# Performance work log

Measured on AMD Instinct MI355X. Metric: run time of the kernel, lower is better.

The kernel has to match this reference:

```python
import jax, jax.numpy as jnp
import numpy as np

# Static module configuration (RT-DETR defaults, 640x640 input pyramid)
SPATIAL_SHAPES = ((80, 80), (40, 40), (20, 20))
N_HEADS = 8
N_LEVELS = 3
N_POINTS = 4
D_MODEL = 256
HEAD_DIM = D_MODEL // N_HEADS
OFFSET_SCALE = 0.5
LP = N_LEVELS * N_POINTS


def setup_inputs() -> dict:
    key = jax.random.key(0)
    ks = jax.random.split(key, 10)
    B, Q = 16, 300
    S = sum(h * w for h, w in SPATIAL_SHAPES)  # 8400

    def w(k, shape, scale=0.02):
        return jax.random.normal(k, shape, jnp.float32) * scale

    return {
        "hidden_states": jax.random.normal(ks[0], (B, Q, D_MODEL), jnp.float32),
        "encoder_hidden_states": jax.random.normal(ks[1], (B, S, D_MODEL), jnp.float32),
        # (cx, cy, w, h) boxes in (0,1); 4-coordinate RTDETRv2 path
        "reference_points": jax.random.uniform(ks[2], (B, Q, 1, 4), jnp.float32, 0.1, 0.9),
        "w_value": w(ks[3], (D_MODEL, D_MODEL)),
        "b_value": jnp.zeros((D_MODEL,), jnp.float32),
        "w_offsets": w(ks[4], (N_HEADS * LP * 2, D_MODEL)),
        "b_offsets": w(ks[5], (N_HEADS * LP * 2,), 0.5),
        "w_attn": w(ks[6], (N_HEADS * LP, D_MODEL)),
        "b_attn": jnp.zeros((N_HEADS * LP,), jnp.float32),
        "w_out": w(ks[7], (D_MODEL, D_MODEL)),
        "b_out": jnp.zeros((D_MODEL,), jnp.float32),
    }


def _bilinear_sample(img, gx, gy):
    """grid_sample(mode=bilinear, padding_mode=zeros, align_corners=False).
    img: [N, C, H, W]; gx, gy: [N, Q, P] absolute pixel coords (already W*loc-0.5).
    Returns [N, Q, P, C]."""
    N, C, H, W = img.shape
    x0 = jnp.floor(gx)
    y0 = jnp.floor(gy)
    x1 = x0 + 1.0
    y1 = y0 + 1.0
    wx1 = gx - x0
    wx0 = 1.0 - wx1
    wy1 = gy - y0
    wy0 = 1.0 - wy1
    b = jnp.arange(N)[:, None, None]

    def gather(ix, iy):
        valid = (ix >= 0) & (ix < W) & (iy >= 0) & (iy < H)
        ixc = jnp.clip(ix, 0, W - 1).astype(jnp.int32)
        iyc = jnp.clip(iy, 0, H - 1).astype(jnp.int32)
        v = img[b, :, iyc, ixc]  # [N,Q,P,C]
        return v * valid[..., None].astype(img.dtype)

    return (gather(x0, y0) * (wx0 * wy0)[..., None]
            + gather(x1, y0) * (wx1 * wy0)[..., None]
            + gather(x0, y1) * (wx0 * wy1)[..., None]
            + gather(x1, y1) * (wx1 * wy1)[..., None])


def _msda_v2(hidden_states, encoder_hidden_states, reference_points,
             w_value, b_value, w_offsets, b_offsets, w_attn, b_attn, w_out, b_out):
    B, Q, _ = hidden_states.shape
    S = encoder_hidden_states.shape[1]

    value = (encoder_hidden_states @ w_value.T + b_value).reshape(B, S, N_HEADS, HEAD_DIM)
    offsets = (hidden_states @ w_offsets.T + b_offsets).reshape(B, Q, N_HEADS, LP, 2)
    attn = jax.nn.softmax(
        (hidden_states @ w_attn.T + b_attn).reshape(B, Q, N_HEADS, LP), axis=-1)

    # n_points_scale = [1/P]*L*P; 4-coordinate reference points (cx,cy,w,h)
    n_points_scale = jnp.float32(1.0 / N_POINTS)
    offset = offsets * n_points_scale * reference_points[:, :, None, :, 2:] * OFFSET_SCALE
    loc = reference_points[:, :, None, :, :2] + offset  # [B,Q,H,LP,2] in (0,1)

    # head-major value: [B*H, hd, S]
    v = value.transpose(0, 2, 3, 1).reshape(B * N_HEADS, HEAD_DIM, S)
    grids = loc.transpose(0, 2, 1, 3, 4).reshape(B * N_HEADS, Q, LP, 2)

    sampled = []
    start = 0
    for lvl, (H, W) in enumerate(SPATIAL_SHAPES):
        vl = v[:, :, start:start + H * W].reshape(B * N_HEADS, HEAD_DIM, H, W)
        g = grids[:, :, lvl * N_POINTS:(lvl + 1) * N_POINTS, :]
        # torch: grid = 2*loc-1 with align_corners=False -> pixel = loc*W - 0.5
        gx = g[..., 0] * W - 0.5
        gy = g[..., 1] * H - 0.5
        sampled.append(_bilinear_sample(vl, gx, gy))  # [B*H, Q, P, hd]
        start += H * W

    sv = jnp.concatenate(sampled, axis=2)  # [B*H, Q, LP, hd]
    aw = attn.transpose(0, 2, 1, 3).reshape(B * N_HEADS, Q, LP, 1)
    out = (sv * aw).sum(axis=2)  # [B*H, Q, hd]
    out = out.reshape(B, N_HEADS, Q, HEAD_DIM).transpose(0, 2, 1, 3).reshape(B, Q, D_MODEL)
    return out @ w_out.T + b_out


def reference(hidden_states, encoder_hidden_states, reference_points,
              w_value, b_value, w_offsets, b_offsets, w_attn, b_attn, w_out, b_out):
    return _msda_v2(hidden_states, encoder_hidden_states, reference_points,
                    w_value, b_value, w_offsets, b_offsets, w_attn, b_attn, w_out, b_out)
```

## Files before the change

### kernel.cpp

```cpp
#include <hip/hip_runtime.h>


typedef __attribute__((ext_vector_type(8))) short short8;
typedef __attribute__((ext_vector_type(4))) float f32x4;

__device__ __forceinline__ unsigned short f2bf(float f) {
    union { float f; unsigned int i; } v; v.f = f;
    unsigned int r = v.i + 0x7FFFu + ((v.i >> 16) & 1u);
    return (unsigned short)(r >> 16);
}
__device__ __forceinline__ float bf2f(unsigned short u) {
    union { unsigned int i; float f; } v;
    v.i = ((unsigned int)u) << 16;
    return v.f;
}
__device__ __forceinline__ unsigned int cvtpk(float lo, float hi) {
    unsigned int r;
    asm("v_cvt_pk_bf16_f32 %0, %1, %2" : "=v"(r) : "v"(lo), "v"(hi));
    return r;
}
__device__ __forceinline__ short8 cvt8(const float* p) {
    f32x4 x = *(const f32x4*)p;
    f32x4 y = *(const f32x4*)(p + 4);
    union { short8 s; unsigned int u[4]; } r;
    r.u[0] = cvtpk(x[0], x[1]);
    r.u[1] = cvtpk(x[2], x[3]);
    r.u[2] = cvtpk(y[0], y[1]);
    r.u[3] = cvtpk(y[2], y[3]);
    return r.s;
}
__device__ __forceinline__ short8 pack8(f32x4 x, f32x4 y) {
    union { short8 s; unsigned int u[4]; } r;
    r.u[0] = cvtpk(x[0], x[1]);
    r.u[1] = cvtpk(x[2], x[3]);
    r.u[2] = cvtpk(y[0], y[1]);
    r.u[3] = cvtpk(y[2], y[3]);
    return r.s;
}
__device__ __forceinline__ void barrier_lgkm() {
    asm volatile("s_waitcnt lgkmcnt(0)\n\ts_barrier" ::: "memory");
}
__device__ __forceinline__ void gload_lds16(const void* g, void* l) {
    __builtin_amdgcn_global_load_lds(
        (const __attribute__((address_space(1))) void*)g,
        (__attribute__((address_space(3))) void*)l, 16, 0, 0);
}

__global__ __launch_bounds__(256) void prep_kernel(
    const float* __restrict__ wv, const float* __restrict__ wo,
    const float* __restrict__ w_off, const float* __restrict__ w_attn,
    short8* __restrict__ wv_s, short8* __restrict__ wo_s, short8* __restrict__ wp_s)
{
    const int blk = blockIdx.x, tid = threadIdx.x;
    if (blk < 64) {
        const float* W = (blk < 32) ? wv : wo;
        short8* out    = (blk < 32) ? wv_s : wo_s;
        int s   = ((blk & 31) << 8) + tid;
        int kcb = s >> 10, sl = s & 1023;
        int n = ((sl >> 6) << 4) + (sl & 15);
        int k = (kcb << 5) + (((sl >> 4) & 3) << 3);
        out[s] = cvt8(W + n * 256 + k);
    } else {
        int s   = ((blk - 64) << 8) + tid;
        int kcb = s / 1152, sl = s - kcb * 1152;
        int n = ((sl >> 6) << 4) + (sl & 15);
        int k = (kcb << 5) + (((sl >> 4) & 3) << 3);
        const float* p = (n < 192) ? (w_off + (size_t)n * 256 + k)
                                   : (w_attn + (size_t)(n - 192) * 256 + k);
        wp_s[s] = cvt8(p);
    }
}

__global__ __launch_bounds__(256) void gemm128(
    const float* __restrict__ A,
    const short8* __restrict__ Wswz,
    const float* __restrict__ bias,
    unsigned short* __restrict__ C)
{
    __shared__ short8 lb[1024];
    const int tid  = threadIdx.x;
    const int wave = tid >> 6;
    const int lane = tid & 63;
    const int row0 = (blockIdx.x >> 1) * 128;
    const int colt = blockIdx.x & 1;
    const int mq   = wave >> 1;
    const int nq   = wave & 1;

    f32x4 acc[4][4];
#pragma unroll
    for (int i = 0; i < 4; ++i)
#pragma unroll
        for (int j = 0; j < 4; ++j) acc[i][j] = (f32x4){0.f, 0.f, 0.f, 0.f};

    const int sa0 = tid, sa1 = tid + 256;
    const int am0 = row0 + ((sa0 >> 6) << 4) + (sa0 & 15);
    const int ak0 = ((sa0 >> 4) & 3) << 3;
    const int am1 = row0 + ((sa1 >> 6) << 4) + (sa1 & 15);
    const int ak1 = ((sa1 >> 4) & 3) << 3;

    const float* pa0 = A + (size_t)am0 * 256 + ak0;
    const float* pa1 = A + (size_t)am1 * 256 + ak1;

    f32x4 a00 = *(const f32x4*)(pa0);
    f32x4 a01 = *(const f32x4*)(pa0 + 4);
    f32x4 a10 = *(const f32x4*)(pa1);
    f32x4 a11 = *(const f32x4*)(pa1 + 4);

    const int wv64 = wave << 6;
    const short8* wcol = Wswz + (colt << 9);
    short8* ldsB0 = &lb[512 + wv64];
    short8* ldsB1 = &lb[768 + wv64];

    for (int kcb = 0; kcb < 8; ++kcb) {
        __builtin_amdgcn_s_barrier();

        lb[sa0] = pack8(a00, a01);
        lb[sa1] = pack8(a10, a11);

        const short8* wsrc = wcol + (kcb << 10) + wv64 + lane;
        gload_lds16(wsrc,       ldsB0);
        gload_lds16(wsrc + 256, ldsB1);
        asm volatile("" ::: "memory");

        if (kcb < 7) {
            const float* q0 = pa0 + ((kcb + 1) << 5);
            const float* q1 = pa1 + ((kcb + 1) << 5);
            a00 = *(const f32x4*)(q0);
            a01 = *(const f32x4*)(q0 + 4);
            a10 = *(const f32x4*)(q1);
            a11 = *(const f32x4*)(q1 + 4);
            asm volatile("s_waitcnt vmcnt(4) lgkmcnt(0)\n\ts_barrier" ::: "memory");
        } else {
            asm volatile("s_waitcnt vmcnt(0) lgkmcnt(0)\n\ts_barrier" ::: "memory");
        }

        short8 af[4], bf[4];
#pragma unroll
        for (int i = 0; i < 4; ++i) af[i] = lb[((mq << 2) + i) * 64 + lane];
#pragma unroll
        for (int j = 0; j < 4; ++j) bf[j] = lb[512 + ((nq << 2) + j) * 64 + lane];
#pragma unroll
        for (int i = 0; i < 4; ++i)
#pragma unroll
            for (int j = 0; j < 4; ++j)
                acc[i][j] = __builtin_amdgcn_mfma_f32_16x16x32_bf16(af[i], bf[j], acc[i][j], 0, 0, 0);
    }

    const int ncol = lane & 15;
    const int rsub = (lane >> 4) << 2;
#pragma unroll
    for (int i = 0; i < 4; ++i) {
        const int rb = row0 + ((mq << 2) + i) * 16 + rsub;
#pragma unroll
        for (int j = 0; j < 4; ++j) {
            const int n = (colt << 7) + ((nq << 2) + j) * 16 + ncol;
            const float bv = bias[n];
            unsigned int d0 = cvtpk(acc[i][j][0] + bv, acc[i][j][1] + bv);
            unsigned int d1 = cvtpk(acc[i][j][2] + bv, acc[i][j][3] + bv);
            C[(size_t)(rb + 0) * 256 + n] = (unsigned short)(d0 & 0xFFFFu);
            C[(size_t)(rb + 1) * 256 + n] = (unsigned short)(d0 >> 16);
            C[(size_t)(rb + 2) * 256 + n] = (unsigned short)(d1 & 0xFFFFu);
            C[(size_t)(rb + 3) * 256 + n] = (unsigned short)(d1 >> 16);
        }
    }
}

template <bool A_BF16, bool OUT_BF16>
__global__ __launch_bounds__(256) void gemm_nt(
    const void* __restrict__ Av,
    const short8* __restrict__ Wswz,
    const float* __restrict__ bias,
    void* __restrict__ Cv)
{
    __shared__ short8 lb[2048];
    const int tid  = threadIdx.x;
    const int wave = tid >> 6;
    const int lane = tid & 63;
    const int row0 = blockIdx.x * 64 + wave * 16;

    f32x4 acc[16];
#pragma unroll
    for (int t = 0; t < 16; ++t) acc[t] = (f32x4){0.f, 0.f, 0.f, 0.f};

    const int am = row0 + (lane & 15);
    const int kq = (lane >> 4) << 3;

    const unsigned short* Ab = (const unsigned short*)Av;
    const float*          Af = (const float*)Av;

    short8 acur[2], anext[2];
#pragma unroll
    for (int kk = 0; kk < 2; ++kk) {
        if (A_BF16) acur[kk] = *(const short8*)(Ab + (size_t)am * 256 + (kk << 5) + kq);
        else        acur[kk] = cvt8(Af + (size_t)am * 256 + (kk << 5) + kq);
    }

    for (int st = 0; st < 4; ++st) {
        barrier_lgkm();
#pragma unroll
        for (int i = 0; i < 8; ++i) {
            int s = tid + (i << 8);
            lb[s] = Wswz[(st << 11) + s];
        }
        barrier_lgkm();

        if (st < 3) {
            int kc = (st + 1) << 6;
#pragma unroll
            for (int kk = 0; kk < 2; ++kk) {
                if (A_BF16) anext[kk] = *(const short8*)(Ab + (size_t)am * 256 + kc + (kk << 5) + kq);
                else        anext[kk] = cvt8(Af + (size_t)am * 256 + kc + (kk << 5) + kq);
            }
        }

#pragma unroll
        for (int t = 0; t < 16; ++t) {
            short8 b0 = lb[t * 64 + lane];
            acc[t] = __builtin_amdgcn_mfma_f32_16x16x32_bf16(acur[0], b0, acc[t], 0, 0, 0);
            short8 b1 = lb[1024 + t * 64 + lane];
            acc[t] = __builtin_amdgcn_mfma_f32_16x16x32_bf16(acur[1], b1, acc[t], 0, 0, 0);
        }
        acur[0] = anext[0];
        acur[1] = anext[1];
    }

    const int ncol = lane & 15;
    const int rb   = row0 + ((lane >> 4) << 2);
#pragma unroll
    for (int t = 0; t < 16; ++t) {
        int n = (t << 4) + ncol;
        float bv = bias[n];
        if (OUT_BF16) {
            unsigned int d0 = cvtpk(acc[t][0] + bv, acc[t][1] + bv);
            unsigned int d1 = cvtpk(acc[t][2] + bv, acc[t][3] + bv);
            ((unsigned short*)Cv)[(size_t)(rb + 0) * 256 + n] = (unsigned short)(d0 & 0xFFFFu);
            ((unsigned short*)Cv)[(size_t)(rb + 1) * 256 + n] = (unsigned short)(d0 >> 16);
            ((unsigned short*)Cv)[(size_t)(rb + 2) * 256 + n] = (unsigned short)(d1 & 0xFFFFu);
            ((unsigned short*)Cv)[(size_t)(rb + 3) * 256 + n] = (unsigned short)(d1 >> 16);
        } else {
#pragma unroll
            for (int r = 0; r < 4; ++r)
                ((float*)Cv)[(size_t)(rb + r) * 256 + n] = acc[t][r] + bv;
        }
    }
}

#define LGS 296
__global__ __launch_bounds__(256) void proj_gemm(
    const float* __restrict__ hidden,
    const short8* __restrict__ Wswz,
    const float* __restrict__ b_off, const float* __restrict__ b_attn,
    const float* __restrict__ refp,
    float* __restrict__ attnw, float* __restrict__ locw)
{
    __shared__ char smem[32 * LGS * 4];
    short8* lb = (short8*)smem;
    float*  lg = (float*)smem;

    const int tid  = threadIdx.x;
    const int wave = tid >> 6;
    const int lane = tid & 63;
    const int rq0  = blockIdx.x * 32;
    const int rg   = wave >> 1;
    const int ts   = (wave & 1) * 9;
    const int row0 = rq0 + rg * 16;

    f32x4 acc[9];
#pragma unroll
    for (int t = 0; t < 9; ++t) acc[t] = (f32x4){0.f, 0.f, 0.f, 0.f};

    const int am = row0 + (lane & 15);
    const int kq = (lane >> 4) << 3;

    for (int kcb = 0; kcb < 8; ++kcb) {
        __syncthreads();
#pragma unroll
        for (int i = 0; i < 5; ++i) {
            int s = tid + (i << 8);
            if (s < 1152) lb[s] = Wswz[kcb * 1152 + s];
        }
        __syncthreads();

        short8 a = cvt8(hidden + (size_t)am * 256 + (kcb << 5) + kq);
#pragma unroll
        for (int t = 0; t < 9; ++t)
            acc[t] = __builtin_amdgcn_mfma_f32_16x16x32_bf16(a, lb[(ts + t) * 64 + lane], acc[t], 0, 0, 0);
    }

    __syncthreads();
    const int ncol = lane & 15;
    const int rb   = rg * 16 + ((lane >> 4) << 2);
#pragma unroll
    for (int t = 0; t < 9; ++t) {
        int n = (ts + t) * 16 + ncol;
        float bv = (n < 192) ? b_off[n] : b_attn[n - 192];
#pragma unroll
        for (int r = 0; r < 4; ++r)
            lg[(rb + r) * LGS + n] = acc[t][r] + bv;
    }
    __syncthreads();

    {
        int r = tid >> 3, h = tid & 7;
        const float* lrow = lg + r * LGS + 192 + h * 12;
        float m = -1e30f;
#pragma unroll
        for (int p = 0; p < 12; ++p) m = fmaxf(m, lrow[p]);
        float e[12], sum = 0.f;
#pragma unroll
        for (int p = 0; p < 12; ++p) { e[p] = __expf(lrow[p] - m); sum += e[p]; }
        float inv = 1.f / sum;
        float* ao = attnw + (size_t)(rq0 + r) * 96 + h * 12;
#pragma unroll
        for (int p = 0; p < 12; ++p) ao[p] = e[p] * inv;
    }
    if (tid < 192) {
        int xy = tid & 1;
        for (int r = 0; r < 32; ++r) {
            int rq = rq0 + r;
            float rc  = refp[(size_t)rq * 4 + xy];
            float rwh = refp[(size_t)rq * 4 + 2 + xy];
            locw[(size_t)rq * 192 + tid] = rc + lg[r * LGS + tid] * 0.125f * rwh;
        }
    }
}

__global__ __launch_bounds__(256) void sample_kernel(
    const unsigned short* __restrict__ value,
    const float* __restrict__ attnw, const float* __restrict__ locw,
    unsigned short* __restrict__ sampled)
{
    const int rq  = blockIdx.x;
    const int b   = rq / 300;
    const int tid = threadIdx.x;

    __shared__ int4   soff[96];
    __shared__ float4 swt[96];

    if (tid < 96) {
        int h = tid / 12, lp = tid - h * 12;
        int l = lp >> 2;
        int Wl = (l == 0) ? 80 : (l == 1) ? 40 : 20;
        int s0 = (l == 0) ? 0  : (l == 1) ? 6400 : 8000;
        float lx = locw[(size_t)rq * 192 + h * 24 + lp * 2];
        float ly = locw[(size_t)rq * 192 + h * 24 + lp * 2 + 1];
        float aw = attnw[(size_t)rq * 96 + h * 12 + lp];
        float gx = lx * (float)Wl - 0.5f;
        float gy = ly * (float)Wl - 0.5f;
        float x0f = floorf(gx), y0f = floorf(gy);
        int   x0 = (int)x0f,   y0 = (int)y0f;
        float wx1 = gx - x0f, wx0 = 1.f - wx1;
        float wy1 = gy - y0f, wy0 = 1.f - wy1;
        int4 of; float4 wt;
#pragma unroll
        for (int j = 0; j < 4; ++j) {
            int x = x0 + (j & 1), y = y0 + (j >> 1);
            bool ok = (x >= 0) & (x < Wl) & (y >= 0) & (y < Wl);
            int idx = ok ? (((b * 8400 + s0 + y * Wl + x) * 8 + h) * 32) : 0;
            float w = ok ? aw * ((j & 1) ? wx1 : wx0) * ((j >> 1) ? wy1 : wy0) : 0.f;
            ((int*)&of)[j] = idx;
            ((float*)&wt)[j] = w;
        }
        soff[tid] = of;
        swt[tid]  = wt;
    }
    __syncthreads();

    const int h = tid >> 5, c = tid & 31;
    float acc = 0.f;
#pragma unroll
    for (int lp = 0; lp < 12; ++lp) {
        int idx = h * 12 + lp;
        int4   of = soff[idx];
        float4 wt = swt[idx];
        acc += wt.x * bf2f(value[of.x + c]);
        acc += wt.y * bf2f(value[of.y + c]);
        acc += wt.z * bf2f(value[of.z + c]);
        acc += wt.w * bf2f(value[of.w + c]);
    }
    sampled[(size_t)rq * 256 + tid] = f2bf(acc);
}

extern "C" void kernel_launch(void* const* d_in, const int* in_sizes, int n_in,
                              void* d_out, int out_size, void* d_ws, size_t ws_size,
                              hipStream_t stream)
{
    const float* hidden  = (const float*)d_in[0];
    const float* enc     = (const float*)d_in[1];
    const float* refp    = (const float*)d_in[2];
    const float* w_value = (const float*)d_in[3];
    const float* b_value = (const float*)d_in[4];
    const float* w_off   = (const float*)d_in[5];
    const float* b_off   = (const float*)d_in[6];
    const float* w_attn  = (const float*)d_in[7];
    const float* b_attn  = (const float*)d_in[8];
    const float* w_out   = (const float*)d_in[9];
    const float* b_out   = (const float*)d_in[10];

    char* ws = (char*)d_ws;
    unsigned short* value   = (unsigned short*)ws;
    unsigned short* sampled = (unsigned short*)(ws + 68812800);
    float*          attnw   = (float*)(ws + 71270400);
    float*          locw    = (float*)(ws + 73113600);
    short8*         wv_swz  = (short8*)(ws + 76800000);
    short8*         wo_swz  = (short8*)(ws + 76931072);
    short8*         wp_swz  = (short8*)(ws + 77062144);

    prep_kernel<<<100, 256, 0, stream>>>(w_value, w_out, w_off, w_attn,
                                         wv_swz, wo_swz, wp_swz);
    gemm128<<<2100, 256, 0, stream>>>(enc, wv_swz, b_value, value);
    proj_gemm<<<150, 256, 0, stream>>>(hidden, wp_swz, b_off, b_attn,
                                       refp, attnw, locw);
    sample_kernel<<<4800, 256, 0, stream>>>(value, attnw, locw, sampled);
    gemm_nt<true, false><<<75, 256, 0, stream>>>(sampled, wo_swz, b_out,
                                                 d_out);
}
```

Measured before the change: 301.9 us.

## Drop LDS staging in value GEMM, swizzle block order, split output GEMM columns

The value-projection GEMM now loads A fragments and pre-swizzled B fragments straight from global memory into registers, with register double-buffering. This replaces LDS staging and its barriers. Blocks are remapped so consecutive groups of 8 row-tiles share a column half, which should improve L2 reuse of A. The output GEMM is split into two column halves per row tile, doubling the grid from 75 to 150 blocks for better CU occupancy, at the cost of reading A twice and each wave loading redundant B fragments.

```diff
diff --git a/kernel.cpp b/kernel.cpp
--- a/kernel.cpp
+++ b/kernel.cpp
@@ -39,11 +39,6 @@
 }
 __device__ __forceinline__ void barrier_lgkm() {
     asm volatile("s_waitcnt lgkmcnt(0)\n\ts_barrier" ::: "memory");
-}
-__device__ __forceinline__ void gload_lds16(const void* g, void* l) {
-    __builtin_amdgcn_global_load_lds(
-        (const __attribute__((address_space(1))) void*)g,
-        (__attribute__((address_space(3))) void*)l, 16, 0, 0);
 }
 
 __global__ __launch_bounds__(256) void prep_kernel(
@@ -77,12 +72,21 @@
     const float* __restrict__ bias,
     unsigned short* __restrict__ C)
 {
-    __shared__ short8 lb[1024];
     const int tid  = threadIdx.x;
     const int wave = tid >> 6;
     const int lane = tid & 63;
-    const int row0 = (blockIdx.x >> 1) * 128;
-    const int colt = blockIdx.x & 1;
+
+    const int g = blockIdx.x;
+    int row_blk, colt;
+    if (g < 2096) {
+        row_blk = ((g >> 4) << 3) + (g & 7);
+        colt    = (g >> 3) & 1;
+    } else {
+        int r = g - 2096;
+        row_blk = 1048 + (r >> 1);
+        colt    = r & 1;
+    }
+    const int row0 = row_blk * 128;
     const int mq   = wave >> 1;
     const int nq   = wave & 1;
 
@@ -92,58 +96,51 @@
 #pragma unroll
         for (int j = 0; j < 4; ++j) acc[i][j] = (f32x4){0.f, 0.f, 0.f, 0.f};
 
-    const int sa0 = tid, sa1 = tid + 256;
-    const int am0 = row0 + ((sa0 >> 6) << 4) + (sa0 & 15);
-    const int ak0 = ((sa0 >> 4) & 3) << 3;
-    const int am1 = row0 + ((sa1 >> 6) << 4) + (sa1 & 15);
-    const int ak1 = ((sa1 >> 4) & 3) << 3;
-
-    const float* pa0 = A + (size_t)am0 * 256 + ak0;
-    const float* pa1 = A + (size_t)am1 * 256 + ak1;
-
-    f32x4 a00 = *(const f32x4*)(pa0);
-    f32x4 a01 = *(const f32x4*)(pa0 + 4);
-    f32x4 a10 = *(const f32x4*)(pa1);
-    f32x4 a11 = *(const f32x4*)(pa1 + 4);
-
-    const int wv64 = wave << 6;
-    const short8* wcol = Wswz + (colt << 9);
-    short8* ldsB0 = &lb[512 + wv64];
-    short8* ldsB1 = &lb[768 + wv64];
-
+    const float* pa[4];
+#pragma unroll
+    for (int i = 0; i < 4; ++i)
+        pa[i] = A + (size_t)(row0 + ((mq << 2) + i) * 16 + (lane & 15)) * 256
+                  + ((lane >> 4) << 3);
+
+    const short8* pb = Wswz + (((colt << 3) + (nq << 2)) << 6) + lane;
+
+    f32x4 a0[4], a1[4];
+    short8 bcur[4], bnext[4];
+#pragma unroll
+    for (int i = 0; i < 4; ++i) {
+        a0[i] = *(const f32x4*)(pa[i]);
+        a1[i] = *(const f32x4*)(pa[i] + 4);
+    }
+#pragma unroll
+    for (int j = 0; j < 4; ++j) bcur[j] = pb[j << 6];
+    pb += 1024;
+
+#pragma unroll
     for (int kcb = 0; kcb < 8; ++kcb) {
-        __builtin_amdgcn_s_barrier();
-
-        lb[sa0] = pack8(a00, a01);
-        lb[sa1] = pack8(a10, a11);
-
-        const short8* wsrc = wcol + (kcb << 10) + wv64 + lane;
-        gload_lds16(wsrc,       ldsB0);
-        gload_lds16(wsrc + 256, ldsB1);
-        asm volatile("" ::: "memory");
+        short8 af[4];
+#pragma unroll
+        for (int i = 0; i < 4; ++i) af[i] = pack8(a0[i], a1[i]);
 
         if (kcb < 7) {
-            const float* q0 = pa0 + ((kcb + 1) << 5);
-            const float* q1 = pa1 + ((kcb + 1) << 5);
-            a00 = *(const f32x4*)(q0);
-            a01 = *(const f32x4*)(q0 + 4);
-            a10 = *(const f32x4*)(q1);
-            a11 = *(const f32x4*)(q1 + 4);
-            asm volatile("s_waitcnt vmcnt(4) lgkmcnt(0)\n\ts_barrier" ::: "memory");
-        } else {
-            asm volatile("s_waitcnt vmcnt(0) lgkmcnt(0)\n\ts_barrier" ::: "memory");
-        }
-
-        short8 af[4], bf[4];
-#pragma unroll
-        for (int i = 0; i < 4; ++i) af[i] = lb[((mq << 2) + i) * 64 + lane];
-#pragma unroll
-        for (int j = 0; j < 4; ++j) bf[j] = lb[512 + ((nq << 2) + j) * 64 + lane];
+            const int ko = (kcb + 1) << 5;
+#pragma unroll
+            for (int i = 0; i < 4; ++i) {
+                a0[i] = *(const f32x4*)(pa[i] + ko);
+                a1[i] = *(const f32x4*)(pa[i] + ko + 4);
+            }
+#pragma unroll
+            for (int j = 0; j < 4; ++j) bnext[j] = pb[j << 6];
+            pb += 1024;
+        }
+
 #pragma unroll
         for (int i = 0; i < 4; ++i)
 #pragma unroll
             for (int j = 0; j < 4; ++j)
-                acc[i][j] = __builtin_amdgcn_mfma_f32_16x16x32_bf16(af[i], bf[j], acc[i][j], 0, 0, 0);
+                acc[i][j] = __builtin_amdgcn_mfma_f32_16x16x32_bf16(af[i], bcur[j], acc[i][j], 0, 0, 0);
+
+#pragma unroll
+        for (int j = 0; j < 4; ++j) bcur[j] = bnext[j];
     }
 
     const int ncol = lane & 15;
@@ -172,15 +169,16 @@
     const float* __restrict__ bias,
     void* __restrict__ Cv)
 {
-    __shared__ short8 lb[2048];
+    __shared__ short8 lb[1024];
     const int tid  = threadIdx.x;
     const int wave = tid >> 6;
     const int lane = tid & 63;
-    const int row0 = blockIdx.x * 64 + wave * 16;
-
-    f32x4 acc[16];
-#pragma unroll
-    for (int t = 0; t < 16; ++t) acc[t] = (f32x4){0.f, 0.f, 0.f, 0.f};
+    const int row0 = (blockIdx.x >> 1) * 64 + wave * 16;
+    const int colt = blockIdx.x & 1;
+
+    f32x4 acc[8];
+#pragma unroll
+    for (int t = 0; t < 8; ++t) acc[t] = (f32x4){0.f, 0.f, 0.f, 0.f};
 
     const int am = row0 + (lane & 15);
     const int kq = (lane >> 4) << 3;
@@ -198,9 +196,10 @@
     for (int st = 0; st < 4; ++st) {
         barrier_lgkm();
 #pragma unroll
-        for (int i = 0; i < 8; ++i) {
-            int s = tid + (i << 8);
-            lb[s] = Wswz[(st << 11) + s];
+        for (int i = 0; i < 4; ++i) {
+            int s  = tid + (i << 8);
+            int kk = s >> 9, r = s & 511;
+            lb[s] = Wswz[(((st << 1) + kk) << 10) + (colt << 9) + r];
         }
         barrier_lgkm();
 
@@ -214,10 +213,10 @@
         }
 
 #pragma unroll
-        for (int t = 0; t < 16; ++t) {
+        for (int t = 0; t < 8; ++t) {
             short8 b0 = lb[t * 64 + lane];
             acc[t] = __builtin_amdgcn_mfma_f32_16x16x32_bf16(acur[0], b0, acc[t], 0, 0, 0);
-            short8 b1 = lb[1024 + t * 64 + lane];
+            short8 b1 = lb[512 + t * 64 + lane];
             acc[t] = __builtin_amdgcn_mfma_f32_16x16x32_bf16(acur[1], b1, acc[t], 0, 0, 0);
         }
         acur[0] = anext[0];
@@ -227,8 +226,8 @@
     const int ncol = lane & 15;
     const int rb   = row0 + ((lane >> 4) << 2);
 #pragma unroll
-    for (int t = 0; t < 16; ++t) {
-        int n = (t << 4) + ncol;
+    for (int t = 0; t < 8; ++t) {
+        int n = (colt << 7) + (t << 4) + ncol;
         float bv = bias[n];
         if (OUT_BF16) {
             unsigned int d0 = cvtpk(acc[t][0] + bv, acc[t][1] + bv);
@@ -412,6 +411,6 @@
     proj_gemm<<<150, 256, 0, stream>>>(hidden, wp_swz, b_off, b_attn,
                                        refp, attnw, locw);
     sample_kernel<<<4800, 256, 0, stream>>>(value, attnw, locw, sampled);
-    gemm_nt<true, false><<<75, 256, 0, stream>>>(sampled, wo_swz, b_out,
-                                                 d_out);
-}
+    gemm_nt<true, false><<<150, 256, 0, stream>>>(sampled, wo_swz, b_out,
+                                                  d_out);
+}
```

Result: slower. 319.9 us (+5.9%).
